# Optimization experiments

Measured on AMD Instinct MI355X. Metric: run time of the kernel, lower is better.

## Reference

```python
import jax, jax.numpy as jnp
import numpy as np

B, D, H, O, E, K = 8192, 1024, 4096, 1024, 8, 2

def setup_inputs() -> dict:
    key = jax.random.key(0)
    ks = jax.random.split(key, 8)
    x = jax.random.normal(ks[0], (B, D), dtype=jnp.float32)
    topk_idx = jax.random.randint(ks[1], (B, K), 0, E, dtype=jnp.int32)
    weights = jax.random.uniform(ks[2], (B, K), dtype=jnp.float32)
    s1 = 1.0 / np.sqrt(D)
    s2 = 1.0 / np.sqrt(H)
    W1 = jax.random.uniform(ks[3], (E, D, H), minval=-s1, maxval=s1, dtype=jnp.float32)
    b1 = jax.random.uniform(ks[4], (E, H), minval=-s1, maxval=s1, dtype=jnp.float32)
    W2 = jax.random.uniform(ks[5], (E, H, O), minval=-s2, maxval=s2, dtype=jnp.float32)
    b2 = jax.random.uniform(ks[6], (E, O), minval=-s2, maxval=s2, dtype=jnp.float32)
    return {"x": x, "topk_idx": topk_idx, "weights": weights,
            "W1": W1, "b1": b1, "W2": W2, "b2": b2}

def reference(x, topk_idx, weights, W1, b1, W2, b2):
    # Per-token gate mass for each expert: gate[b,e] = sum_i weights[b,i]*[topk_idx[b,i]==e]
    # Equivalent to the original masked gather/scatter combine (duplicates in topk_idx sum).
    out = jnp.zeros((x.shape[0], W2.shape[-1]), dtype=x.dtype)
    for e in range(W1.shape[0]):  # small fixed loop over experts
        gate_e = jnp.sum(weights * (topk_idx == e), axis=1)  # [B]
        h = jax.nn.relu(x @ W1[e] + b1[e])                   # [B,H]
        out_e = h @ W2[e] + b2[e]                            # [B,O]
        out = out + gate_e[:, None] * out_e
    return out
```

## Files before the change

### kernel.cpp

```cpp
#include <hip/hip_runtime.h>
#include <stdint.h>

#define B_TOK 8192
#define D_DIM 1024
#define H_DIM 4096
#define O_DIM 1024
#define E_NUM 8
#define K_TOP 2
#define NPAIR (B_TOK * K_TOP)

typedef short bf16x8 __attribute__((ext_vector_type(8)));
typedef float f32x4 __attribute__((ext_vector_type(4)));

struct Hdr {
    int counts[8];
    int offsets[9];
    int total1, total2;
    int base1[9];
    int base2[9];
};

__device__ __forceinline__ unsigned short f2bf(float f) {
    union { float f; unsigned int u; } v; v.f = f;
    unsigned int u = v.u;
    unsigned int r = (u + 0x7fffu + ((u >> 16) & 1u)) >> 16;
    return (unsigned short)r;
}

__device__ __forceinline__ float bf2f(unsigned short s) {
    union { unsigned int u; float f; } v;
    v.u = ((unsigned int)s) << 16;
    return v.f;
}

__device__ __forceinline__ void async16(const void* g, const void* l) {
    __builtin_amdgcn_global_load_lds(
        (__attribute__((address_space(1))) void*)(uintptr_t)g,
        (__attribute__((address_space(3))) void*)(uint32_t)(uintptr_t)l,
        16, 0, 0);
}


__global__ void cvt_x_kernel(const float* __restrict__ x, unsigned short* __restrict__ xb) {
    int i = (blockIdx.x * 256 + threadIdx.x) * 4;
    float4 v = *(const float4*)(x + i);
    ushort4 o;
    o.x = f2bf(v.x); o.y = f2bf(v.y); o.z = f2bf(v.z); o.w = f2bf(v.w);
    *(ushort4*)(xb + i) = o;
}

__global__ __launch_bounds__(256) void tconv2_kernel(const float* __restrict__ W1,
                                                     const float* __restrict__ W2,
                                                     unsigned short* __restrict__ o1,
                                                     unsigned short* __restrict__ o2) {
    __shared__ unsigned short tb[64 * 68];
    int z = blockIdx.y;
    int bid = blockIdx.x;
    int R, C, c0, r0;
    const float* ip;
    unsigned short* op;
    if (z < 8) {
        R = D_DIM; C = H_DIM;
        c0 = (bid & 63) * 64; r0 = (bid >> 6) * 64;
        ip = W1 + (size_t)z * R * C;
        op = o1 + (size_t)z * R * C;
    } else {
        R = H_DIM; C = O_DIM;
        c0 = (bid & 15) * 64; r0 = (bid >> 4) * 64;
        ip = W2 + (size_t)(z - 8) * R * C;
        op = o2 + (size_t)(z - 8) * R * C;
    }
    int tid = threadIdx.x;
    int lr = tid >> 4;
    int lc = (tid & 15) * 4;
#pragma unroll
    for (int i = 0; i < 4; i++) {
        int row = lr + i * 16;
        float4 v = *(const float4*)&ip[(size_t)(r0 + row) * C + c0 + lc];
        ushort4 o;
        o.x = f2bf(v.x); o.y = f2bf(v.y); o.z = f2bf(v.z); o.w = f2bf(v.w);
        *(ushort4*)&tb[row * 68 + lc] = o;
    }
    __syncthreads();
#pragma unroll
    for (int i = 0; i < 4; i++) {
        int c = lr + i * 16;
        ushort4 o;
        o.x = tb[(lc + 0) * 68 + c];
        o.y = tb[(lc + 1) * 68 + c];
        o.z = tb[(lc + 2) * 68 + c];
        o.w = tb[(lc + 3) * 68 + c];
        *(ushort4*)&op[(size_t)(c0 + c) * R + r0 + lc] = o;
    }
}


__global__ __launch_bounds__(1024) void route_kernel(const int* __restrict__ topk,
                                                     Hdr* hdr,
                                                     int* __restrict__ ptok,
                                                     int* __restrict__ pslot) {
    __shared__ int wcnt[16][8];
    __shared__ int wcur[16][8];
    int tid = threadIdx.x;
    int w = tid >> 6;
    if ((tid & 63) < 8) wcnt[w][tid & 63] = 0;
    __syncthreads();
    int ev[16];
#pragma unroll
    for (int j = 0; j < 16; j++) {
        ev[j] = topk[tid + j * 1024];
        atomicAdd(&wcnt[w][ev[j]], 1);
    }
    __syncthreads();
    if (tid == 0) {
        int off = 0, t1 = 0, t2 = 0;
        for (int e = 0; e < 8; e++) {
            int c = 0;
            for (int w2 = 0; w2 < 16; w2++) {
                wcur[w2][e] = off + c;
                c += wcnt[w2][e];
            }
            hdr->counts[e] = c;
            hdr->offsets[e] = off;
            hdr->base1[e] = t1;
            hdr->base2[e] = t2;
            t1 += ((c + 255) >> 8) * (H_DIM / 256);
            t2 += ((c + 127) >> 7) * (O_DIM / 128);
            off += c;
        }
        hdr->offsets[8] = off;
        hdr->base1[8] = t1;
        hdr->base2[8] = t2;
        hdr->total1 = t1;
        hdr->total2 = t2;
    }
    __syncthreads();
#pragma unroll
    for (int j = 0; j < 16; j++) {
        int i = tid + j * 1024;
        int pos = atomicAdd(&wcur[w][ev[j]], 1);
        ptok[pos] = i >> 1;
        pslot[i] = pos;
    }
}

__global__ void ws_fail_kernel(float* out) { out[0] = 1.0e9f; }


#define ASL(BUF, KH) ((BUF) * 32768 + (KH) * 16384)

#define STG_A(BUF, KH, KOFF) do { \
    async16(Ab + srcA[0] + (KOFF), smem + ASL(BUF, KH) + wu * 2048); \
    async16(Ab + srcA[1] + (KOFF), smem + ASL(BUF, KH) + wu * 2048 + 1024); } while (0)

#define STG_B(BUF, KH, KOFF) do { \
    async16(Bb + srcB[0] + (KOFF), smem + 65536 + ASL(BUF, KH) + wu * 2048); \
    async16(Bb + srcB[1] + (KOFF), smem + 65536 + ASL(BUF, KH) + wu * 2048 + 1024); } while (0)

#define VM6 asm volatile("s_waitcnt vmcnt(6)" ::: "memory")
#define VM0 asm volatile("s_waitcnt vmcnt(0)" ::: "memory")
#define NOPX ((void)0)

#define PHASE0(BUF, KH, STAGE, CKPT) do { \
    STAGE; \
    bq[0] = *(const bf16x8*)&smem[pBo[0] + ASL(BUF, KH)]; \
    bq[1] = *(const bf16x8*)&smem[pBo[1] + ASL(BUF, KH)]; \
    bq[2] = *(const bf16x8*)&smem[pBo[2] + ASL(BUF, KH)]; \
    bq[3] = *(const bf16x8*)&smem[pBo[3] + ASL(BUF, KH)]; \
    aq[0] = *(const bf16x8*)&smem[pAo[0] + ASL(BUF, KH)]; \
    aq[1] = *(const bf16x8*)&smem[pAo[1] + ASL(BUF, KH)]; \
    aq[2] = *(const bf16x8*)&smem[pAo[2] + ASL(BUF, KH)]; \
    aq[3] = *(const bf16x8*)&smem[pAo[3] + ASL(BUF, KH)]; \
    __builtin_amdgcn_s_barrier(); \
    asm volatile("s_waitcnt lgkmcnt(0)" ::: "memory"); \
    __builtin_amdgcn_s_setprio(1); \
    _Pragma("unroll") \
    for (int q_ = 0; q_ < 4; ++q_) { \
        _Pragma("unroll") \
        for (int n_ = 0; n_ < 4; ++n_) \
            acc[q_][n_] = __builtin_amdgcn_mfma_f32_16x16x32_bf16(aq[q_], bq[n_], acc[q_][n_], 0, 0, 0); \
    } \
    __builtin_amdgcn_s_setprio(0); \
    CKPT; \
    __builtin_amdgcn_s_barrier(); \
} while (0)

#define PHASE1(BUF, KH, STAGE, CKPT) do { \
    STAGE; \
    aq[0] = *(const bf16x8*)&smem[pAo[4] + ASL(BUF, KH)]; \
    aq[1] = *(const bf16x8*)&smem[pAo[5] + ASL(BUF, KH)]; \
    aq[2] = *(const bf16x8*)&smem[pAo[6] + ASL(BUF, KH)]; \
    aq[3] = *(const bf16x8*)&smem[pAo[7] + ASL(BUF, KH)]; \
    __builtin_amdgcn_s_barrier(); \
    asm volatile("s_waitcnt lgkmcnt(0)" ::: "memory"); \
    __builtin_amdgcn_s_setprio(1); \
    _Pragma("unroll") \
    for (int q_ = 0; q_ < 4; ++q_) { \
        _Pragma("unroll") \
        for (int n_ = 0; n_ < 4; ++n_) \
            acc[4 + q_][n_] = __builtin_amdgcn_mfma_f32_16x16x32_bf16(aq[q_], bq[n_], acc[4 + q_][n_], 0, 0, 0); \
    } \
    __builtin_amdgcn_s_setprio(0); \
    CKPT; \
    __builtin_amdgcn_s_barrier(); \
} while (0)

template <int KD, int N, bool GATHER>
__global__ __launch_bounds__(512, 2) void moe_gemm256_kernel(
    const unsigned short* __restrict__ A,
    const unsigned short* __restrict__ Bt,
    const float* __restrict__ bias,
    const Hdr* __restrict__ hdr,
    const int* __restrict__ ptok,
    unsigned short* __restrict__ outp) {

    extern __shared__ __align__(16) char smem[];
    constexpr int NT = KD / 64;
    constexpr int NI = NT / 2;
    static_assert(NT >= 4 && (NT % 2) == 0, "K-tile count");

    const int tid = threadIdx.x;
    const int lane = tid & 63;
    const int wv = tid >> 6;
    const int wu = __builtin_amdgcn_readfirstlane(wv);
    const int lr = lane & 15;
    const int lkg = lane >> 4;
    const int wr = wv >> 2;
    const int wc = wv & 3;

    const int total = hdr->total1;
    const int* tb = hdr->base1;

    int chunk = (total + 7) >> 3;
    int seq = (blockIdx.x & 7) * chunk + (blockIdx.x >> 3);
    if (seq >= total) return;

    int e = 0;
#pragma unroll
    for (int j = 1; j < 8; j++)
        if (seq >= tb[j]) e = j;
    e = __builtin_amdgcn_readfirstlane(e);
    int lt = seq - tb[e];
    int cnt = hdr->counts[e], off = hdr->offsets[e];
    int MT = (cnt + 255) >> 8;
    int mtile = lt % MT, ntile = lt / MT;
    int m0 = mtile * 256, n0 = ntile * 256;

    const char* Ab = (const char*)A;
    const char* Bb = (const char*)(Bt + (size_t)e * ((size_t)N * KD));

    uint32_t srcA[2], srcB[2];
#pragma unroll
    for (int l = 0; l < 2; ++l) {
        int g = wv * 128 + l * 64 + lane;
        int rp = g >> 2, cp = g & 3;
        int c = (cp - (rp >> 1)) & 3;
        int q = off + m0 + rp;
        q = q > NPAIR - 1 ? NPAIR - 1 : q;
        uint32_t rowA = GATHER ? (uint32_t)ptok[q] : (uint32_t)q;
        srcA[l] = rowA * (uint32_t)(KD * 2) + (uint32_t)(c * 16);
        srcB[l] = (uint32_t)(n0 + rp) * (uint32_t)(KD * 2) + (uint32_t)(c * 16);
    }

    uint32_t pAo[8], pBo[4];
#pragma unroll
    for (int mr = 0; mr < 8; ++mr) {
        int r = wr * 128 + mr * 16 + lr;
        pAo[mr] = (uint32_t)(r * 64 + ((lkg + (r >> 1)) & 3) * 16);
    }
#pragma unroll
    for (int nr = 0; nr < 4; ++nr) {
        int r = wc * 64 + nr * 16 + lr;
        pBo[nr] = (uint32_t)(65536 + r * 64 + ((lkg + (r >> 1)) & 3) * 16);
    }

    f32x4 acc[8][4];
#pragma unroll
    for (int i = 0; i < 8; ++i)
#pragma unroll
        for (int j = 0; j < 4; ++j)
            acc[i][j] = (f32x4){0.f, 0.f, 0.f, 0.f};
    bf16x8 aq[4], bq[4];

    STG_A(0, 0, 0u);   STG_B(0, 0, 0u);
    STG_A(0, 1, 64u);  STG_B(0, 1, 64u);
    STG_A(1, 0, 128u); STG_B(1, 0, 128u);
    STG_B(1, 1, 192u);
    VM0;
    __builtin_amdgcn_s_barrier();

    for (int it = 0; it < NI - 1; ++it) {
        const uint32_t kb = (uint32_t)it * 256u;
        PHASE0(0, 0, STG_A(1, 1, kb + 192u), NOPX);
        PHASE1(0, 0, STG_B(0, 0, kb + 256u), NOPX);
        PHASE0(0, 1, STG_A(0, 0, kb + 256u), NOPX);
        PHASE1(0, 1, STG_B(0, 1, kb + 320u), VM6);
        PHASE0(1, 0, STG_A(0, 1, kb + 320u), NOPX);
        PHASE1(1, 0, STG_B(1, 0, kb + 384u), NOPX);
        PHASE0(1, 1, STG_A(1, 0, kb + 384u), NOPX);
        PHASE1(1, 1, STG_B(1, 1, kb + 448u), VM6);
    }
    {
        const uint32_t kb = (uint32_t)(NI - 1) * 256u;
        PHASE0(0, 0, STG_A(1, 1, kb + 192u), NOPX);
        PHASE1(0, 0, NOPX, NOPX);
        PHASE0(0, 1, NOPX, NOPX);
        PHASE1(0, 1, NOPX, VM0);
        PHASE0(1, 0, NOPX, NOPX);
        PHASE1(1, 0, NOPX, NOPX);
        PHASE0(1, 1, NOPX, NOPX);
        PHASE1(1, 1, NOPX, NOPX);
    }

    unsigned short* eb = (unsigned short*)smem;
    int rows_valid = cnt - m0;
    if (rows_valid > 256) rows_valid = 256;
#pragma unroll
    for (int pass = 0; pass < 2; ++pass) {
        __syncthreads();
        if (wr == pass) {
#pragma unroll
            for (int nr = 0; nr < 4; ++nr) {
                int n = wc * 64 + nr * 16 + lr;
                float bv = bias[(size_t)e * N + n0 + n];
#pragma unroll
                for (int mr = 0; mr < 8; ++mr) {
#pragma unroll
                    for (int r2 = 0; r2 < 4; ++r2) {
                        int ml = mr * 16 + lkg * 4 + r2;
                        float v = acc[mr][nr][r2] + bv;
                        if (GATHER) v = v > 0.f ? v : 0.f;
                        eb[ml * 264 + n] = f2bf(v);
                    }
                }
            }
        }
        __syncthreads();
        int rv = rows_valid - pass * 128;
        if (rv > 128) rv = 128;
#pragma unroll
        for (int j = 0; j < 8; ++j) {
            int idx = j * 512 + tid;
            int row = idx >> 5;
            int c16 = idx & 31;
            if (row < rv) {
                uint4 v = *(const uint4*)&eb[row * 264 + c16 * 8];
                *(uint4*)&outp[(size_t)(off + m0 + pass * 128 + row) * N + n0 + c16 * 8] = v;
            }
        }
    }
}

template <int K, int N, bool GATHER>
__global__ __launch_bounds__(256, 4) void moe_gemm128_kernel(
    const unsigned short* __restrict__ A,
    const unsigned short* __restrict__ Bt,
    const float* __restrict__ bias,
    const Hdr* __restrict__ hdr,
    const int* __restrict__ ptok,
    unsigned short* __restrict__ outp) {

    __shared__ __align__(16) unsigned short smem[128 * 132];
    unsigned short* As = smem;
    unsigned short* Bs = smem + 128 * 64;

    const int tid = threadIdx.x;
    const int lane = tid & 63;
    const int wv = tid >> 6;
    const int wu = __builtin_amdgcn_readfirstlane(wv);
    const int wm = (wv & 1) * 64;
    const int wn = (wv >> 1) * 64;
    const int lr = lane & 15;
    const int lkg = lane >> 4;

    const int total = hdr->total2;
    const int* tb = hdr->base2;
    constexpr int NT = N / 128;

    int chunk = (total + 7) >> 3;
    int seq = (blockIdx.x & 7) * chunk + (blockIdx.x >> 3);
    if (seq >= total) return;

    int e = 0;
#pragma unroll
    for (int j = 1; j < 8; j++)
        if (seq >= tb[j]) e = j;
    e = __builtin_amdgcn_readfirstlane(e);
    int lt = seq - tb[e];
    int cnt = hdr->counts[e], off = hdr->offsets[e];
    int MT = (cnt + 127) >> 7;

    int band = lt / (NT * 8);
    int r = lt - band * (NT * 8);
    int mrem = MT - band * 8;
    mrem = mrem > 8 ? 8 : mrem;
    int gsz = mrem * 8;
    int g = r / gsz;
    int rg = r - g * gsz;
    int gm = rg % mrem;
    int gn = rg / mrem;
    int mtile = band * 8 + gm;
    int ntile = g * 8 + gn;
    int m0 = mtile * 128, n0 = ntile * 128;

    const char* Ab = (const char*)A;
    const char* Bb = (const char*)(Bt + (size_t)e * ((size_t)N * K));
    uint32_t offA[4], offB[4];
#pragma unroll
    for (int i = 0; i < 4; i++) {
        int s = i * 256 + tid;
        int rr = s >> 3;
        int cl = (s & 7) ^ (rr & 7);
        int p = off + m0 + rr;
        p = p > NPAIR - 1 ? NPAIR - 1 : p;
        uint32_t row = GATHER ? (uint32_t)ptok[p] : (uint32_t)p;
        offA[i] = (row * (uint32_t)K + (uint32_t)cl * 8u) * 2u;
        offB[i] = (((uint32_t)(n0 + rr)) * (uint32_t)K + (uint32_t)cl * 8u) * 2u;
    }

    f32x4 zero = {0.f, 0.f, 0.f, 0.f};
    f32x4 acc[4][4];
#pragma unroll
    for (int mt = 0; mt < 4; mt++)
#pragma unroll
        for (int nt = 0; nt < 4; nt++) acc[mt][nt] = zero;

    for (int k0 = 0; k0 < K; k0 += 64) {
#pragma unroll
        for (int i = 0; i < 4; i++) {
            async16(Ab + offA[i], &As[(i * 256 + wu * 64) * 8]);
            async16(Bb + offB[i], &Bs[(i * 256 + wu * 64) * 8]);
            offA[i] += 128;
            offB[i] += 128;
        }
        __syncthreads();
#pragma unroll
        for (int ks = 0; ks < 2; ks++) {
            bf16x8 af[4];
#pragma unroll
            for (int q = 0; q < 4; q++) {
                int ra = wm + q * 16 + lr;
                int ca = (ks * 4 + lkg) ^ (ra & 7);
                af[q] = *(const bf16x8*)&As[ra * 64 + ca * 8];
            }
#pragma unroll
            for (int nt = 0; nt < 4; nt++) {
                int rb = wn + nt * 16 + lr;
                int cb = (ks * 4 + lkg) ^ (rb & 7);
                bf16x8 bfr = *(const bf16x8*)&Bs[rb * 64 + cb * 8];
#pragma unroll
                for (int mt = 0; mt < 4; mt++)
                    acc[mt][nt] = __builtin_amdgcn_mfma_f32_16x16x32_bf16(
                        af[mt], bfr, acc[mt][nt], 0, 0, 0);
            }
        }
        __syncthreads();
    }

#pragma unroll
    for (int nt = 0; nt < 4; nt++) {
        int n = wn + nt * 16 + lr;
        float bv = bias[(size_t)e * N + n0 + n];
#pragma unroll
        for (int mt = 0; mt < 4; mt++) {
#pragma unroll
            for (int r2 = 0; r2 < 4; r2++) {
                int m = wm + mt * 16 + lkg * 4 + r2;
                float v = acc[mt][nt][r2] + bv;
                if (GATHER) v = v > 0.f ? v : 0.f;
                smem[m * 132 + n] = f2bf(v);
            }
        }
    }
    __syncthreads();
    int rows_valid = cnt - m0;
    if (rows_valid > 128) rows_valid = 128;
#pragma unroll
    for (int j = 0; j < 16; j++) {
        int idx = j * 256 + tid;
        int row = idx >> 5;
        int lc8 = idx & 31;
        if (row < rows_valid) {
            uint2 v = *(const uint2*)&smem[row * 132 + lc8 * 4];
            *(uint2*)&outp[(size_t)(off + m0 + row) * N + n0 + lc8 * 4] = v;
        }
    }
}

__global__ void combine_kernel(const unsigned short* __restrict__ oslot,
                               const int* __restrict__ pslot,
                               const float* __restrict__ wts,
                               float* __restrict__ out) {
    int tok = blockIdx.x;
    int s0 = pslot[tok * 2], s1 = pslot[tok * 2 + 1];
    float g0 = wts[tok * 2], g1 = wts[tok * 2 + 1];
    int n = threadIdx.x * 4;
    ushort4 a = *(const ushort4*)&oslot[(size_t)s0 * O_DIM + n];
    ushort4 b = *(const ushort4*)&oslot[(size_t)s1 * O_DIM + n];
    float4 o;
    o.x = g0 * bf2f(a.x) + g1 * bf2f(b.x);
    o.y = g0 * bf2f(a.y) + g1 * bf2f(b.y);
    o.z = g0 * bf2f(a.z) + g1 * bf2f(b.z);
    o.w = g0 * bf2f(a.w) + g1 * bf2f(b.w);
    *(float4*)&out[(size_t)tok * O_DIM + n] = o;
}


extern "C" void kernel_launch(void* const* d_in, const int* in_sizes, int n_in,
                              void* d_out, int out_size, void* d_ws, size_t ws_size,
                              hipStream_t stream) {
    const float* x   = (const float*)d_in[0];
    const int* topk  = (const int*)d_in[1];
    const float* wts = (const float*)d_in[2];
    const float* W1  = (const float*)d_in[3];
    const float* b1  = (const float*)d_in[4];
    const float* W2  = (const float*)d_in[5];
    const float* b2  = (const float*)d_in[6];
    float* out = (float*)d_out;

    char* ws = (char*)d_ws;
    size_t off = 0;
    auto alloc = [&](size_t bytes) -> void* {
        void* p = ws + off;
        off += (bytes + 255) & ~(size_t)255;
        return p;
    };
    Hdr* hdr = (Hdr*)alloc(sizeof(Hdr));
    int* ptok = (int*)alloc((size_t)NPAIR * 4);
    int* pslot = (int*)alloc((size_t)NPAIR * 4);
    unsigned short* xb   = (unsigned short*)alloc((size_t)B_TOK * D_DIM * 2);
    unsigned short* W1bt = (unsigned short*)alloc((size_t)E_NUM * D_DIM * H_DIM * 2);
    unsigned short* W2bt = (unsigned short*)alloc((size_t)E_NUM * H_DIM * O_DIM * 2);
    unsigned short* hbuf = (unsigned short*)alloc((size_t)NPAIR * H_DIM * 2);
    unsigned short* oslot = W1bt;

    if (off > ws_size) {
        hipMemsetAsync(d_out, 0, (size_t)out_size * sizeof(float), stream);
        ws_fail_kernel<<<1, 1, 0, stream>>>(out);
        return;
    }

    static int attr_done = 0;
    if (!attr_done) {
        (void)hipFuncSetAttribute(
            reinterpret_cast<const void*>(&moe_gemm256_kernel<D_DIM, H_DIM, true>),
            hipFuncAttributeMaxDynamicSharedMemorySize, 131072);
        attr_done = 1;
    }

    cvt_x_kernel<<<(B_TOK * D_DIM) / 1024, 256, 0, stream>>>(x, xb);
    tconv2_kernel<<<dim3(1024, 16, 1), 256, 0, stream>>>(W1, W2, W1bt, W2bt);
    route_kernel<<<1, 1024, 0, stream>>>(topk, hdr, ptok, pslot);

    moe_gemm256_kernel<D_DIM, H_DIM, true><<<1152, 512, 131072, stream>>>(
        xb, W1bt, b1, hdr, ptok, hbuf);
    moe_gemm128_kernel<H_DIM, O_DIM, false><<<1152, 256, 0, stream>>>(
        hbuf, W2bt, b2, hdr, ptok, oslot);
    combine_kernel<<<B_TOK, 256, 0, stream>>>(oslot, pslot, wts, out);
}
```

Baseline: 718.7 us.

## Split expert GEMMs into two N-half launches and widen weight transpose tiles

Each grouped GEMM now runs as two launches. Each launch only handles tiles whose N index falls in one half, so the concurrently active weight working set is halved and should stay in cache. The weight convert-transpose kernel now uses 128x64 tiles: it writes transposed bf16 into LDS on load and emits 16-byte vector stores. The risks are extra launch overhead, a tail at each launch boundary, and idle blocks that start and exit early.

```diff
diff --git a/kernel.cpp b/kernel.cpp
--- a/kernel.cpp
+++ b/kernel.cpp
@@ -53,44 +53,45 @@
                                                      const float* __restrict__ W2,
                                                      unsigned short* __restrict__ o1,
                                                      unsigned short* __restrict__ o2) {
-    __shared__ unsigned short tb[64 * 68];
+    __shared__ unsigned short tb[64 * 134];
     int z = blockIdx.y;
     int bid = blockIdx.x;
-    int R, C, c0, r0;
+    int R, C;
     const float* ip;
     unsigned short* op;
     if (z < 8) {
         R = D_DIM; C = H_DIM;
-        c0 = (bid & 63) * 64; r0 = (bid >> 6) * 64;
         ip = W1 + (size_t)z * R * C;
         op = o1 + (size_t)z * R * C;
     } else {
         R = H_DIM; C = O_DIM;
-        c0 = (bid & 15) * 64; r0 = (bid >> 4) * 64;
         ip = W2 + (size_t)(z - 8) * R * C;
         op = o2 + (size_t)(z - 8) * R * C;
     }
+    int tR = R >> 7;
+    int r0 = (bid % tR) * 128;
+    int c0 = (bid / tR) * 64;
     int tid = threadIdx.x;
-    int lr = tid >> 4;
-    int lc = (tid & 15) * 4;
+
+    int rl = tid >> 4;
+    int cg = (tid & 15) * 4;
+#pragma unroll
+    for (int p = 0; p < 8; p++) {
+        int r = rl + p * 16;
+        float4 v = *(const float4*)&ip[(size_t)(r0 + r) * C + c0 + cg];
+        tb[(cg + 0) * 134 + r] = f2bf(v.x);
+        tb[(cg + 1) * 134 + r] = f2bf(v.y);
+        tb[(cg + 2) * 134 + r] = f2bf(v.z);
+        tb[(cg + 3) * 134 + r] = f2bf(v.w);
+    }
+    __syncthreads();
+
+    int r16 = (tid & 15) * 8;
 #pragma unroll
     for (int i = 0; i < 4; i++) {
-        int row = lr + i * 16;
-        float4 v = *(const float4*)&ip[(size_t)(r0 + row) * C + c0 + lc];
-        ushort4 o;
-        o.x = f2bf(v.x); o.y = f2bf(v.y); o.z = f2bf(v.z); o.w = f2bf(v.w);
-        *(ushort4*)&tb[row * 68 + lc] = o;
-    }
-    __syncthreads();
-#pragma unroll
-    for (int i = 0; i < 4; i++) {
-        int c = lr + i * 16;
-        ushort4 o;
-        o.x = tb[(lc + 0) * 68 + c];
-        o.y = tb[(lc + 1) * 68 + c];
-        o.z = tb[(lc + 2) * 68 + c];
-        o.w = tb[(lc + 3) * 68 + c];
-        *(ushort4*)&op[(size_t)(c0 + c) * R + r0 + lc] = o;
+        int c = (tid >> 4) + i * 16;
+        uint4 v = *(const uint4*)&tb[c * 134 + r16];
+        *(uint4*)&op[(size_t)(c0 + c) * R + r0 + r16] = v;
     }
 }
 
@@ -212,7 +213,8 @@
     const float* __restrict__ bias,
     const Hdr* __restrict__ hdr,
     const int* __restrict__ ptok,
-    unsigned short* __restrict__ outp) {
+    unsigned short* __restrict__ outp,
+    int phase) {
 
     extern __shared__ __align__(16) char smem[];
     constexpr int NT = KD / 64;
@@ -244,6 +246,7 @@
     int cnt = hdr->counts[e], off = hdr->offsets[e];
     int MT = (cnt + 255) >> 8;
     int mtile = lt % MT, ntile = lt / MT;
+    if ((ntile >> 3) != phase) return;
     int m0 = mtile * 256, n0 = ntile * 256;
 
     const char* Ab = (const char*)A;
@@ -358,7 +361,8 @@
     const float* __restrict__ bias,
     const Hdr* __restrict__ hdr,
     const int* __restrict__ ptok,
-    unsigned short* __restrict__ outp) {
+    unsigned short* __restrict__ outp,
+    int phase) {
 
     __shared__ __align__(16) unsigned short smem[128 * 132];
     unsigned short* As = smem;
@@ -401,6 +405,7 @@
     int gn = rg / mrem;
     int mtile = band * 8 + gm;
     int ntile = g * 8 + gn;
+    if ((ntile >> 2) != phase) return;
     int m0 = mtile * 128, n0 = ntile * 128;
 
     const char* Ab = (const char*)A;
@@ -549,12 +554,16 @@
     }
 
     cvt_x_kernel<<<(B_TOK * D_DIM) / 1024, 256, 0, stream>>>(x, xb);
-    tconv2_kernel<<<dim3(1024, 16, 1), 256, 0, stream>>>(W1, W2, W1bt, W2bt);
+    tconv2_kernel<<<dim3(512, 16, 1), 256, 0, stream>>>(W1, W2, W1bt, W2bt);
     route_kernel<<<1, 1024, 0, stream>>>(topk, hdr, ptok, pslot);
 
     moe_gemm256_kernel<D_DIM, H_DIM, true><<<1152, 512, 131072, stream>>>(
-        xb, W1bt, b1, hdr, ptok, hbuf);
+        xb, W1bt, b1, hdr, ptok, hbuf, 0);
+    moe_gemm256_kernel<D_DIM, H_DIM, true><<<1152, 512, 131072, stream>>>(
+        xb, W1bt, b1, hdr, ptok, hbuf, 1);
     moe_gemm128_kernel<H_DIM, O_DIM, false><<<1152, 256, 0, stream>>>(
-        hbuf, W2bt, b2, hdr, ptok, oslot);
+        hbuf, W2bt, b2, hdr, ptok, oslot, 0);
+    moe_gemm128_kernel<H_DIM, O_DIM, false><<<1152, 256, 0, stream>>>(
+        hbuf, W2bt, b2, hdr, ptok, oslot, 1);
     combine_kernel<<<B_TOK, 256, 0, stream>>>(oslot, pslot, wts, out);
 }
```

Measured after the change: 754.1 us. 1.05x slower.
